# Optimization experiments

Hardware: AMD Instinct MI355X
Metric: run time of the kernel (lower is better)

The kernel has to match this reference:

```python
import jax, jax.numpy as jnp
import numpy as np
from jax import lax

B, C, T, S = 32, 122, 500, 13
WID, EMB, PROJ = 80, 8, 1024
HID = 768  # (H=1)*(W=96)*(E=8) after CNN
EPS = 1e-5
DN = ('NCHW', 'OIHW', 'NCHW')


def setup_inputs() -> dict:
    key = jax.random.key(0)
    ks = jax.random.split(key, 24)
    f32 = jnp.float32
    def n(k, shape, scale):
        return (jax.random.normal(k, shape, dtype=f32) * scale).astype(f32)
    return {
        'x': jax.random.normal(ks[0], (B, C, T), dtype=f32),
        'subject_ids': jax.random.randint(ks[1], (B,), 0, S, dtype=jnp.int32),
        'W_sub': n(ks[2], (S, T, T), 0.04),      # nn.Linear(500,500) weight per subject
        'b_sub': n(ks[3], (S, T), 0.02),
        'conv1_w': n(ks[4], (WID, 1, 1, 5), 0.3),
        'conv1_b': n(ks[5], (WID,), 0.02),
        'bn1_g': 1.0 + n(ks[6], (WID,), 0.1),
        'bn1_b': n(ks[7], (WID,), 0.1),
        'bn1_m': n(ks[8], (WID,), 0.1),
        'bn1_v': 0.5 + jax.random.uniform(ks[9], (WID,), dtype=f32),
        'conv2_w': n(ks[10], (WID, WID, C, 1), 0.01),
        'conv2_b': n(ks[11], (WID,), 0.02),
        'bn2_g': 1.0 + n(ks[12], (WID,), 0.1),
        'bn2_b': n(ks[13], (WID,), 0.1),
        'bn2_m': n(ks[14], (WID,), 0.1),
        'bn2_v': 0.5 + jax.random.uniform(ks[15], (WID,), dtype=f32),
        'proj_w': n(ks[16], (EMB, WID, 1, 1), 0.1),
        'proj_b': n(ks[17], (EMB,), 0.02),
        'mlp1_w': n(ks[18], (PROJ, HID), 0.03),
        'mlp1_b': n(ks[19], (PROJ,), 0.02),
        'mlp2_w': n(ks[20], (PROJ, PROJ), 0.03),
        'mlp2_b': n(ks[21], (PROJ,), 0.02),
        'ln_g': 1.0 + n(ks[22], (PROJ,), 0.05),
        'ln_b': n(ks[23], (PROJ,), 0.05),
    }


def _bn(h, g, b, m, v):
    # eval-mode BatchNorm2d over channel axis 1
    scale = (g / jnp.sqrt(v + EPS))[None, :, None, None]
    shift = (b - m * g / jnp.sqrt(v + EPS))[None, :, None, None]
    return h * scale + shift


def _forward(x, subject_ids, W_sub, b_sub, conv1_w, conv1_b, bn1_g, bn1_b, bn1_m, bn1_v,
             conv2_w, conv2_b, bn2_g, bn2_b, bn2_m, bn2_v, proj_w, proj_b,
             mlp1_w, mlp1_b, mlp2_w, mlp2_b, ln_g, ln_b):
    # --- per-subject routing: gather each sample's Linear(500,500) and apply ---
    Wg = W_sub[subject_ids]                       # [B,T,T] (out,in)
    bg = b_sub[subject_ids]                       # [B,T]
    out = jnp.einsum('bcs,bts->bct', x, Wg) + bg[:, None, :]
    # --- spatio-temporal CNN (eval mode: dropout = identity) ---
    h = out[:, None, :, :]                        # [B,1,C,T]
    h = lax.conv_general_dilated(h, conv1_w, (1, 1), 'VALID', dimension_numbers=DN)
    h = h + conv1_b[None, :, None, None]          # [B,80,122,496]
    h = lax.reduce_window(h, 0.0, lax.add, (1, 1, 1, 17), (1, 1, 1, 5), 'VALID') / 17.0  # [B,80,122,96]
    h = jax.nn.elu(_bn(h, bn1_g, bn1_b, bn1_m, bn1_v))
    h = lax.conv_general_dilated(h, conv2_w, (1, 1), 'VALID', dimension_numbers=DN)
    h = h + conv2_b[None, :, None, None]          # [B,80,1,96]
    h = jax.nn.elu(_bn(h, bn2_g, bn2_b, bn2_m, bn2_v))
    h = lax.conv_general_dilated(h, proj_w, (1, 1), 'VALID', dimension_numbers=DN)
    h = h + proj_b[None, :, None, None]           # [B,8,1,96]
    z = jnp.transpose(h, (0, 2, 3, 1)).reshape(h.shape[0], -1)  # [B,768]
    # --- MLP projector: Linear -> Residual(GELU+Linear) -> LayerNorm ---
    z1 = z @ mlp1_w.T + mlp1_b                    # [B,1024]
    r = jax.nn.gelu(z1, approximate=False) @ mlp2_w.T + mlp2_b
    y = z1 + r
    mu = jnp.mean(y, axis=-1, keepdims=True)
    var = jnp.var(y, axis=-1, keepdims=True)
    return (y - mu) / jnp.sqrt(var + EPS) * ln_g + ln_b


def reference(x, subject_ids, W_sub, b_sub, conv1_w, conv1_b, bn1_g, bn1_b, bn1_m, bn1_v,
              conv2_w, conv2_b, bn2_g, bn2_b, bn2_m, bn2_v, proj_w, proj_b,
              mlp1_w, mlp1_b, mlp2_w, mlp2_b, ln_g, ln_b):
    return _forward(x, subject_ids, W_sub, b_sub, conv1_w, conv1_b, bn1_g, bn1_b, bn1_m, bn1_v,
                    conv2_w, conv2_b, bn2_g, bn2_b, bn2_m, bn2_v, proj_w, proj_b,
                    mlp1_w, mlp1_b, mlp2_w, mlp2_b, ln_g, ln_b)
```

## Files before the change

### kernel.cpp

```cpp
#include <hip/hip_runtime.h>
#include <math.h>

#define BB 32
#define CC 122
#define TT 500
#define SS 13
#define WID 80
#define EMB 8
#define PROJ 1024
#define HID 768
#define TP 96
#define EPSF 1e-5f
#define KP 9760
#define KBN 305
#define KSPLIT 16

typedef float f32x4 __attribute__((ext_vector_type(4)));
typedef __bf16 bf16x8 __attribute__((ext_vector_type(8)));
typedef unsigned short u16x8 __attribute__((ext_vector_type(8)));
union BF8 { u16x8 u; bf16x8 b; };

__device__ __forceinline__ unsigned short f2bf(float f) {
    union { float f; unsigned u; } v; v.f = f;
    unsigned r = v.u + 0x7FFFu + ((v.u >> 16) & 1u);
    return (unsigned short)(r >> 16);
}

__device__ __forceinline__ float eluf(float x) {
    return x > 0.f ? x : __expf(x) - 1.f;
}

#define OFF_E    ((size_t)0)
#define OFF_XB   ((size_t)1952000)
#define OFF_WB   ((size_t)3000576)
#define OFF_W2P  ((size_t)4704512)
#define OFF_P    ((size_t)5094912)
#define OFF_PART ((size_t)20086272)
#define OFF_Z    ((size_t)24018432)
#define OFF_Z1   ((size_t)24030720)
#define OFF_G    ((size_t)24063488)
#define OFF_Y    ((size_t)24079872)
#define OFF_W1B  ((size_t)24112640)
#define OFF_W2B  ((size_t)24505856)
#define OFF_WCB  ((size_t)25030144)
#define OFF_B1F  ((size_t)25031424)
#define OFF_SC2  ((size_t)25031504)
#define OFF_SH2  ((size_t)25031584)

#define NPK_X  (2097152)
#define NPK_W  (3407872)
#define NPK_W2 (780800)
#define NPK_M1 (786432)
#define NPK_M2 (1048576)
#define NPK_TOT (NPK_X + NPK_W + NPK_W2 + NPK_M1 + NPK_M2)

__global__ __launch_bounds__(256) void k_pack(const float* __restrict__ x,
                                              const float* __restrict__ W_sub,
                                              const float* __restrict__ conv2_w,
                                              const float* __restrict__ mlp1_w,
                                              const float* __restrict__ mlp2_w,
                                              const float* __restrict__ conv1_w, const float* __restrict__ conv1_b,
                                              const float* __restrict__ g1, const float* __restrict__ b1,
                                              const float* __restrict__ m1, const float* __restrict__ v1,
                                              const float* __restrict__ conv2_b, const float* __restrict__ g2,
                                              const float* __restrict__ b2, const float* __restrict__ m2,
                                              const float* __restrict__ v2,
                                              unsigned short* __restrict__ xb,
                                              unsigned short* __restrict__ wb,
                                              unsigned short* __restrict__ w2p,
                                              unsigned short* __restrict__ w1b,
                                              unsigned short* __restrict__ w2b,
                                              unsigned short* __restrict__ wcb, float* __restrict__ bias1f,
                                              float* __restrict__ scale2, float* __restrict__ shift2f) {
    if (blockIdx.x == 0) {
        int o = threadIdx.x;
        if (o < WID) {
            float s1 = g1[o] * rsqrtf(v1[o] + EPSF);
            float sh1 = b1[o] - m1[o] * s1;
            #pragma unroll
            for (int d = 0; d < 21; d++) {
                int klo = d - 16; if (klo < 0) klo = 0;
                int khi = d;      if (khi > 4) khi = 4;
                float acc = 0.f;
                for (int k = klo; k <= khi; k++) acc += conv1_w[o*5 + k];
                wcb[o*32 + d] = f2bf(acc * s1 * (1.f/17.f));
            }
            #pragma unroll
            for (int d = 21; d < 32; d++) wcb[o*32 + d] = 0;
            bias1f[o] = conv1_b[o] * s1 + sh1;
            float s2 = g2[o] * rsqrtf(v2[o] + EPSF);
            scale2[o] = s2;
            shift2f[o] = conv2_b[o] * s2 + (b2[o] - m2[o] * s2);
        }
    }
    size_t idx = (size_t)blockIdx.x * 256 + threadIdx.x;
    if (idx >= (size_t)NPK_TOT) return;
    if (idx < NPK_X) {
        int s = idx & 511, c = (idx >> 9) & 127, b = idx >> 16;
        float v = (c < CC && s < TT) ? x[((size_t)b * CC + c) * TT + s] : 0.f;
        xb[idx] = f2bf(v);
    } else if (idx < NPK_X + NPK_W) {
        size_t j = idx - NPK_X;
        int s = j & 511, t = (j >> 9) & 511, sub = j >> 18;
        float v = (t < TT && s < TT) ? W_sub[((size_t)sub * TT + t) * TT + s] : 0.f;
        wb[j] = f2bf(v);
    } else if (idx < NPK_X + NPK_W + NPK_W2) {
        size_t j = idx - NPK_X - NPK_W;
        int o = (int)(j / KP);
        int k = (int)(j % KP);
        int c = k / WID, op = k % WID;
        w2p[j] = f2bf(conv2_w[((size_t)(o * WID + op)) * CC + c]);
    } else if (idx < NPK_X + NPK_W + NPK_W2 + NPK_M1) {
        size_t j = idx - NPK_X - NPK_W - NPK_W2;
        w1b[j] = f2bf(mlp1_w[j]);
    } else {
        size_t j = idx - NPK_X - NPK_W - NPK_W2 - NPK_M1;
        w2b[j] = f2bf(mlp2_w[j]);
    }
}

__global__ __launch_bounds__(256) void k_einsum(const unsigned short* __restrict__ xb,
                                                const unsigned short* __restrict__ wb,
                                                const int* __restrict__ sid,
                                                const float* __restrict__ b_sub,
                                                float* __restrict__ oute) {
    int t0 = blockIdx.x * 64, b = blockIdx.y;
    int s = sid[b];
    int tid = threadIdx.x, w = tid >> 6, lr = tid & 15, lg = (tid >> 4) & 3;
    const unsigned short* A0 = xb + ((size_t)(b * 128 + w * 32 + lr)) * 512 + 8 * lg;
    const unsigned short* Bb = wb + (size_t)s * 262144 + 8 * lg;
    f32x4 acc[2][4] = {};
    for (int kb = 0; kb < 512; kb += 32) {
        BF8 a0, a1;
        a0.u = *(const u16x8*)(A0 + kb);
        a1.u = *(const u16x8*)(A0 + 16 * 512 + kb);
        #pragma unroll
        for (int nt = 0; nt < 4; nt++) {
            BF8 bf; bf.u = *(const u16x8*)(Bb + (size_t)(t0 + nt * 16 + lr) * 512 + kb);
            acc[0][nt] = __builtin_amdgcn_mfma_f32_16x16x32_bf16(a0.b, bf.b, acc[0][nt], 0, 0, 0);
            acc[1][nt] = __builtin_amdgcn_mfma_f32_16x16x32_bf16(a1.b, bf.b, acc[1][nt], 0, 0, 0);
        }
    }
    const float* bg = b_sub + (size_t)s * TT;
    #pragma unroll
    for (int nt = 0; nt < 4; nt++) {
        int t = t0 + nt * 16 + lr;
        if (t < TT) {
            float bias = bg[t];
            #pragma unroll
            for (int mt = 0; mt < 2; mt++) {
                int crow = w * 32 + mt * 16 + 4 * lg;
                #pragma unroll
                for (int r = 0; r < 4; r++) {
                    int c = crow + r;
                    if (c < CC) oute[((size_t)b * CC + c) * TT + t] = acc[mt][nt][r] + bias;
                }
            }
        }
    }
}

__global__ __launch_bounds__(256) void k_fir2(const float* __restrict__ oute,
                                              const unsigned short* __restrict__ wcb,
                                              const float* __restrict__ b1f,
                                              unsigned short* __restrict__ p2) {
    __shared__ float e2[2][512];
    __shared__ unsigned short pt[96][164];
    int cp = blockIdx.x, b = blockIdx.y;
    int tid = threadIdx.x;
    int w = tid >> 6, lr = tid & 15, lg = (tid >> 4) & 3;
    if (tid < 250) {
        int cc = tid / 125, i = tid % 125;
        ((float4*)e2[cc])[i] = ((const float4*)(oute + ((size_t)b * CC + cp * 2 + cc) * TT))[i];
    }
    if (tid >= 232) {
        int j = tid - 232; int cc = j / 12, i = 500 + (j % 12);
        e2[cc][i] = 0.f;
    }
    BF8 af[5]; float4 bf4[5];
    #pragma unroll
    for (int ot = 0; ot < 5; ot++) {
        af[ot].u = *(const u16x8*)(wcb + (ot * 16 + lr) * 32 + 8 * lg);
        bf4[ot] = *(const float4*)(b1f + ot * 16 + 4 * lg);
    }
    __syncthreads();
    #pragma unroll
    for (int ui = 0; ui < 3; ui++) {
        int u = w + 4 * ui;
        int cc = u / 6, tt = u % 6;
        int t = tt * 16 + lr;
        const float* ew = e2[cc] + 5 * t + 8 * lg;
        BF8 bfr;
        #pragma unroll
        for (int j = 0; j < 8; j++) bfr.u[j] = f2bf(ew[j]);
        f32x4 acc[5] = {};
        #pragma unroll
        for (int ot = 0; ot < 5; ot++)
            acc[ot] = __builtin_amdgcn_mfma_f32_16x16x32_bf16(af[ot].b, bfr.b, acc[ot], 0, 0, 0);
        #pragma unroll
        for (int ot = 0; ot < 5; ot++) {
            union { unsigned short s[4]; uint2 v; } pk;
            #pragma unroll
            for (int r = 0; r < 4; r++) pk.s[r] = f2bf(eluf(acc[ot][r] + bf4[ot][r]));
            *(uint2*)&pt[t][cc * 80 + ot * 16 + 4 * lg] = pk.v;
        }
    }
    __syncthreads();
    const size_t base = ((size_t)b * KBN + 5 * (size_t)cp) * 3072;
    int q = 2 * tid;
    int l = q >> 3, jj = q & 7;
    int prow_lo = l & 15;
    int pcol_off = ((l >> 4) << 3) + jj;
    #pragma unroll
    for (int r = 0; r < 30; r++) {
        int kbl = r / 6, tt2 = r % 6;
        unsigned v = *(const unsigned*)&pt[tt2 * 16 + prow_lo][kbl * 32 + pcol_off];
        *(unsigned*)(p2 + base + (size_t)(kbl * 6 + tt2) * 512 + q) = v;
    }
}

__global__ __launch_bounds__(384) void k_conv2(const unsigned short* __restrict__ p2,
                                               const unsigned short* __restrict__ w2p,
                                               float* __restrict__ part) {
    int chunk = blockIdx.x, b = blockIdx.y;
    int tid = threadIdx.x, w = tid >> 6, l = tid & 63, lr = l & 15, lg = l >> 4;
    int kb0 = (chunk * KBN) / KSPLIT;
    int kb1 = ((chunk + 1) * KBN) / KSPLIT;
    const unsigned short* Bp = p2 + (size_t)b * KBN * 3072 + (size_t)w * 512 + (size_t)l * 8;
    const unsigned short* Arow = w2p + (size_t)lr * KP + 8 * lg;
    f32x4 acc[5] = {};
    for (int kb = kb0; kb < kb1; kb++) {
        BF8 bf; bf.u = *(const u16x8*)(Bp + (size_t)kb * 3072);
        int ko = kb * 32;
        #pragma unroll
        for (int mt = 0; mt < 5; mt++) {
            BF8 af; af.u = *(const u16x8*)(Arow + (size_t)mt * 16 * KP + ko);
            acc[mt] = __builtin_amdgcn_mfma_f32_16x16x32_bf16(af.b, bf.b, acc[mt], 0, 0, 0);
        }
    }
    float* pp = part + ((size_t)(chunk * BB + b) * WID) * TP;
    int t = w * 16 + lr;
    #pragma unroll
    for (int mt = 0; mt < 5; mt++) {
        int ob = mt * 16 + 4 * lg;
        #pragma unroll
        for (int r = 0; r < 4; r++)
            pp[(size_t)(ob + r) * TP + t] = acc[mt][r];
    }
}

__global__ __launch_bounds__(256) void k_redproj(const float* __restrict__ part,
                                                 const float* __restrict__ scale2,
                                                 const float* __restrict__ shift2f,
                                                 const float* __restrict__ pw,
                                                 const float* __restrict__ pb,
                                                 unsigned short* __restrict__ zbf) {
    __shared__ float ly[WID * TP];
    __shared__ float lw[EMB * WID];
    int b = blockIdx.x, tid = threadIdx.x;
    for (int i = tid; i < EMB * WID; i += 256) lw[i] = pw[i];
    for (int i = tid; i < WID * TP; i += 256) {
        float acc = 0.f;
        #pragma unroll
        for (int ks = 0; ks < KSPLIT; ks++)
            acc += part[(size_t)(ks * BB + b) * (WID * TP) + i];
        int o = i / TP;
        ly[i] = eluf(acc * scale2[o] + shift2f[o]);
    }
    __syncthreads();
    #pragma unroll
    for (int rep = 0; rep < 3; rep++) {
        int j = tid + 256 * rep;
        int e = j & 7, t = j >> 3;
        float acc = pb[e];
        #pragma unroll 10
        for (int o = 0; o < WID; o++) acc = fmaf(ly[o * TP + t], lw[e * WID + o], acc);
        zbf[(size_t)b * HID + j] = f2bf(acc);
    }
}

__global__ __launch_bounds__(256) void k_mlp1(const unsigned short* __restrict__ zbf,
                                              const unsigned short* __restrict__ w1b,
                                              const float* __restrict__ bias,
                                              float* __restrict__ z1,
                                              unsigned short* __restrict__ gbf) {
    __shared__ float accb[2][64][4];
    int tid = threadIdx.x, w = tid >> 6, l = tid & 63, lr = l & 15, lg = l >> 4;
    int mt = w & 1, kh = w >> 1;
    int pcol = blockIdx.x * 16 + lr;
    const unsigned short* wr = w1b + (size_t)pcol * HID + kh * 384 + 8 * lg;
    const unsigned short* za = zbf + (size_t)(mt * 16 + lr) * HID + kh * 384 + 8 * lg;
    f32x4 acc = {};
    for (int kb = 0; kb < 384; kb += 32) {
        BF8 bf; bf.u = *(const u16x8*)(wr + kb);
        BF8 a;  a.u  = *(const u16x8*)(za + kb);
        acc = __builtin_amdgcn_mfma_f32_16x16x32_bf16(a.b, bf.b, acc, 0, 0, 0);
    }
    if (kh == 1) {
        #pragma unroll
        for (int r = 0; r < 4; r++) accb[mt][l][r] = acc[r];
    }
    __syncthreads();
    if (kh == 0) {
        float bs = bias[pcol];
        #pragma unroll
        for (int r = 0; r < 4; r++) {
            int row = mt * 16 + 4 * lg + r;
            float v = acc[r] + accb[mt][l][r] + bs;
            z1[(size_t)row * PROJ + pcol] = v;
            gbf[(size_t)row * PROJ + pcol] = f2bf(0.5f * v * (1.f + erff(v * 0.70710678118654752f)));
        }
    }
}

__global__ __launch_bounds__(256) void k_mlp2(const unsigned short* __restrict__ gbf,
                                              const float* __restrict__ z1,
                                              const unsigned short* __restrict__ w2b,
                                              const float* __restrict__ bias,
                                              float* __restrict__ y) {
    __shared__ float accb[2][64][4];
    int tid = threadIdx.x, w = tid >> 6, l = tid & 63, lr = l & 15, lg = l >> 4;
    int mt = w & 1, kh = w >> 1;
    int q = blockIdx.x * 16 + lr;
    const unsigned short* wr = w2b + (size_t)q * PROJ + kh * 512 + 8 * lg;
    const unsigned short* ga = gbf + (size_t)(mt * 16 + lr) * PROJ + kh * 512 + 8 * lg;
    f32x4 acc = {};
    for (int kb = 0; kb < 512; kb += 32) {
        BF8 bf; bf.u = *(const u16x8*)(wr + kb);
        BF8 a;  a.u  = *(const u16x8*)(ga + kb);
        acc = __builtin_amdgcn_mfma_f32_16x16x32_bf16(a.b, bf.b, acc, 0, 0, 0);
    }
    if (kh == 1) {
        #pragma unroll
        for (int r = 0; r < 4; r++) accb[mt][l][r] = acc[r];
    }
    __syncthreads();
    if (kh == 0) {
        float bs = bias[q];
        #pragma unroll
        for (int r = 0; r < 4; r++) {
            int row = mt * 16 + 4 * lg + r;
            y[(size_t)row * PROJ + q] = acc[r] + accb[mt][l][r] + bs + z1[(size_t)row * PROJ + q];
        }
    }
}

__global__ __launch_bounds__(256) void k_ln(const float* __restrict__ y,
                                            const float* __restrict__ lg,
                                            const float* __restrict__ lb,
                                            float* __restrict__ out) {
    int b = blockIdx.x, tid = threadIdx.x;
    const float4* yr = (const float4*)(y + (size_t)b * PROJ);
    float4 v = yr[tid];
    float s  = v.x + v.y + v.z + v.w;
    float sq = v.x*v.x + v.y*v.y + v.z*v.z + v.w*v.w;
    #pragma unroll
    for (int off = 32; off > 0; off >>= 1) {
        s  += __shfl_down(s, off);
        sq += __shfl_down(sq, off);
    }
    __shared__ float ss[4], ssq[4];
    int wv = tid >> 6, lane = tid & 63;
    if (lane == 0) { ss[wv] = s; ssq[wv] = sq; }
    __syncthreads();
    __shared__ float smu, sinv;
    if (tid == 0) {
        float Sm = ss[0] + ss[1] + ss[2] + ss[3];
        float Sq = ssq[0] + ssq[1] + ssq[2] + ssq[3];
        float mu = Sm * (1.f / PROJ);
        float var = Sq * (1.f / PROJ) - mu * mu;
        smu = mu;
        sinv = rsqrtf(var + EPSF);
    }
    __syncthreads();
    float mu = smu, inv = sinv;
    float4 g4 = ((const float4*)lg)[tid];
    float4 b4 = ((const float4*)lb)[tid];
    float4 o4;
    o4.x = (v.x - mu) * inv * g4.x + b4.x;
    o4.y = (v.y - mu) * inv * g4.y + b4.y;
    o4.z = (v.z - mu) * inv * g4.z + b4.z;
    o4.w = (v.w - mu) * inv * g4.w + b4.w;
    ((float4*)(out + (size_t)b * PROJ))[tid] = o4;
}

extern "C" void kernel_launch(void* const* d_in, const int* in_sizes, int n_in,
                              void* d_out, int out_size, void* d_ws, size_t ws_size,
                              hipStream_t stream) {
    const float* x        = (const float*)d_in[0];
    const int*   sid      = (const int*)  d_in[1];
    const float* W_sub    = (const float*)d_in[2];
    const float* b_sub    = (const float*)d_in[3];
    const float* conv1_w  = (const float*)d_in[4];
    const float* conv1_b  = (const float*)d_in[5];
    const float* bn1_g    = (const float*)d_in[6];
    const float* bn1_b    = (const float*)d_in[7];
    const float* bn1_m    = (const float*)d_in[8];
    const float* bn1_v    = (const float*)d_in[9];
    const float* conv2_w  = (const float*)d_in[10];
    const float* conv2_b  = (const float*)d_in[11];
    const float* bn2_g    = (const float*)d_in[12];
    const float* bn2_b    = (const float*)d_in[13];
    const float* bn2_m    = (const float*)d_in[14];
    const float* bn2_v    = (const float*)d_in[15];
    const float* proj_w   = (const float*)d_in[16];
    const float* proj_b   = (const float*)d_in[17];
    const float* mlp1_w   = (const float*)d_in[18];
    const float* mlp1_b   = (const float*)d_in[19];
    const float* mlp2_w   = (const float*)d_in[20];
    const float* mlp2_b   = (const float*)d_in[21];
    const float* ln_g     = (const float*)d_in[22];
    const float* ln_b     = (const float*)d_in[23];
    float* out = (float*)d_out;
    float* ws  = (float*)d_ws;

    float* ws_e    = ws + OFF_E;
    unsigned short* ws_xb  = (unsigned short*)(ws + OFF_XB);
    unsigned short* ws_wb  = (unsigned short*)(ws + OFF_WB);
    unsigned short* ws_w2p = (unsigned short*)(ws + OFF_W2P);
    unsigned short* ws_p2  = (unsigned short*)(ws + OFF_P);
    float* ws_part = ws + OFF_PART;
    unsigned short* ws_zbf = (unsigned short*)(ws + OFF_Z);
    float* ws_z1   = ws + OFF_Z1;
    unsigned short* ws_gbf = (unsigned short*)(ws + OFF_G);
    float* ws_y    = ws + OFF_Y;
    unsigned short* ws_w1b = (unsigned short*)(ws + OFF_W1B);
    unsigned short* ws_w2b = (unsigned short*)(ws + OFF_W2B);
    unsigned short* ws_wcb = (unsigned short*)(ws + OFF_WCB);
    float* ws_b1f  = ws + OFF_B1F;
    float* ws_sc2  = ws + OFF_SC2;
    float* ws_sh2  = ws + OFF_SH2;

    hipLaunchKernelGGL(k_pack, dim3((NPK_TOT + 255) / 256), dim3(256), 0, stream,
                       x, W_sub, conv2_w, mlp1_w, mlp2_w,
                       conv1_w, conv1_b, bn1_g, bn1_b, bn1_m, bn1_v,
                       conv2_b, bn2_g, bn2_b, bn2_m, bn2_v,
                       ws_xb, ws_wb, ws_w2p, ws_w1b, ws_w2b,
                       ws_wcb, ws_b1f, ws_sc2, ws_sh2);

    hipLaunchKernelGGL(k_einsum, dim3(8, BB), dim3(256), 0, stream,
                       ws_xb, ws_wb, sid, b_sub, ws_e);

    hipLaunchKernelGGL(k_fir2, dim3(CC / 2, BB), dim3(256), 0, stream,
                       ws_e, ws_wcb, ws_b1f, ws_p2);

    hipLaunchKernelGGL(k_conv2, dim3(KSPLIT, BB), dim3(384), 0, stream,
                       ws_p2, ws_w2p, ws_part);

    hipLaunchKernelGGL(k_redproj, dim3(BB), dim3(256), 0, stream,
                       ws_part, ws_sc2, ws_sh2, proj_w, proj_b, ws_zbf);

    hipLaunchKernelGGL(k_mlp1, dim3(PROJ / 16), dim3(256), 0, stream,
                       ws_zbf, ws_w1b, mlp1_b, ws_z1, ws_gbf);

    hipLaunchKernelGGL(k_mlp2, dim3(PROJ / 16), dim3(256), 0, stream,
                       ws_gbf, ws_z1, ws_w2b, mlp2_b, ws_y);

    hipLaunchKernelGGL(k_ln, dim3(BB), dim3(256), 0, stream,
                       ws_y, ln_g, ln_b, out);
}
```

Measured before the change: 221.8 us.

## Fuse reduce/projection, MLP and LayerNorm tail into one kernel with grid barriers

```diff
diff --git a/kernel.cpp b/kernel.cpp
--- a/kernel.cpp
+++ b/kernel.cpp
@@ -14,6 +14,7 @@
 #define KP 9760
 #define KBN 305
 #define KSPLIT 16
+#define NTAIL 64
 
 typedef float f32x4 __attribute__((ext_vector_type(4)));
 typedef __bf16 bf16x8 __attribute__((ext_vector_type(8)));
@@ -37,7 +38,6 @@
 #define OFF_P    ((size_t)5094912)
 #define OFF_PART ((size_t)20086272)
 #define OFF_Z    ((size_t)24018432)
-#define OFF_Z1   ((size_t)24030720)
 #define OFF_G    ((size_t)24063488)
 #define OFF_Y    ((size_t)24079872)
 #define OFF_W1B  ((size_t)24112640)
@@ -46,6 +46,7 @@
 #define OFF_B1F  ((size_t)25031424)
 #define OFF_SC2  ((size_t)25031504)
 #define OFF_SH2  ((size_t)25031584)
+#define OFF_CNT  ((size_t)25031664)
 
 #define NPK_X  (2097152)
 #define NPK_W  (3407872)
@@ -71,9 +72,11 @@
                                               unsigned short* __restrict__ w1b,
                                               unsigned short* __restrict__ w2b,
                                               unsigned short* __restrict__ wcb, float* __restrict__ bias1f,
-                                              float* __restrict__ scale2, float* __restrict__ shift2f) {
+                                              float* __restrict__ scale2, float* __restrict__ shift2f,
+                                              unsigned* __restrict__ bar) {
     if (blockIdx.x == 0) {
         int o = threadIdx.x;
+        if (o < 8) bar[o] = 0u;
         if (o < WID) {
             float s1 = g1[o] * rsqrtf(v1[o] + EPSF);
             float sh1 = b1[o] - m1[o] * s1;
@@ -249,139 +252,153 @@
     }
 }
 
-__global__ __launch_bounds__(256) void k_redproj(const float* __restrict__ part,
-                                                 const float* __restrict__ scale2,
-                                                 const float* __restrict__ shift2f,
-                                                 const float* __restrict__ pw,
-                                                 const float* __restrict__ pb,
-                                                 unsigned short* __restrict__ zbf) {
+__device__ __forceinline__ void gbarrier(unsigned* ctr) {
+    __threadfence();
+    __syncthreads();
+    if (threadIdx.x == 0) {
+        atomicAdd(ctr, 1u);
+        while (atomicAdd(ctr, 0u) < NTAIL) {}
+    }
+    __syncthreads();
+    __threadfence();
+}
+
+__global__ __launch_bounds__(256) void k_tail(const float* __restrict__ part,
+                                              const float* __restrict__ scale2,
+                                              const float* __restrict__ shift2f,
+                                              const float* __restrict__ pw,
+                                              const float* __restrict__ pb,
+                                              const unsigned short* __restrict__ w1b,
+                                              const float* __restrict__ b1m,
+                                              const unsigned short* __restrict__ w2b,
+                                              const float* __restrict__ b2m,
+                                              const float* __restrict__ lg_,
+                                              const float* __restrict__ lb_,
+                                              unsigned short* __restrict__ zbf,
+                                              unsigned short* __restrict__ gbf,
+                                              float* __restrict__ y,
+                                              float* __restrict__ out,
+                                              unsigned* __restrict__ bar) {
     __shared__ float ly[WID * TP];
     __shared__ float lw[EMB * WID];
-    int b = blockIdx.x, tid = threadIdx.x;
-    for (int i = tid; i < EMB * WID; i += 256) lw[i] = pw[i];
-    for (int i = tid; i < WID * TP; i += 256) {
-        float acc = 0.f;
-        #pragma unroll
-        for (int ks = 0; ks < KSPLIT; ks++)
-            acc += part[(size_t)(ks * BB + b) * (WID * TP) + i];
-        int o = i / TP;
-        ly[i] = eluf(acc * scale2[o] + shift2f[o]);
-    }
-    __syncthreads();
-    #pragma unroll
-    for (int rep = 0; rep < 3; rep++) {
-        int j = tid + 256 * rep;
-        int e = j & 7, t = j >> 3;
-        float acc = pb[e];
-        #pragma unroll 10
-        for (int o = 0; o < WID; o++) acc = fmaf(ly[o * TP + t], lw[e * WID + o], acc);
-        zbf[(size_t)b * HID + j] = f2bf(acc);
-    }
-}
-
-__global__ __launch_bounds__(256) void k_mlp1(const unsigned short* __restrict__ zbf,
-                                              const unsigned short* __restrict__ w1b,
-                                              const float* __restrict__ bias,
-                                              float* __restrict__ z1,
-                                              unsigned short* __restrict__ gbf) {
     __shared__ float accb[2][64][4];
     int tid = threadIdx.x, w = tid >> 6, l = tid & 63, lr = l & 15, lg = l >> 4;
     int mt = w & 1, kh = w >> 1;
-    int pcol = blockIdx.x * 16 + lr;
-    const unsigned short* wr = w1b + (size_t)pcol * HID + kh * 384 + 8 * lg;
-    const unsigned short* za = zbf + (size_t)(mt * 16 + lr) * HID + kh * 384 + 8 * lg;
-    f32x4 acc = {};
-    for (int kb = 0; kb < 384; kb += 32) {
-        BF8 bf; bf.u = *(const u16x8*)(wr + kb);
-        BF8 a;  a.u  = *(const u16x8*)(za + kb);
-        acc = __builtin_amdgcn_mfma_f32_16x16x32_bf16(a.b, bf.b, acc, 0, 0, 0);
-    }
-    if (kh == 1) {
-        #pragma unroll
-        for (int r = 0; r < 4; r++) accb[mt][l][r] = acc[r];
-    }
-    __syncthreads();
-    if (kh == 0) {
-        float bs = bias[pcol];
-        #pragma unroll
-        for (int r = 0; r < 4; r++) {
-            int row = mt * 16 + 4 * lg + r;
-            float v = acc[r] + accb[mt][l][r] + bs;
-            z1[(size_t)row * PROJ + pcol] = v;
-            gbf[(size_t)row * PROJ + pcol] = f2bf(0.5f * v * (1.f + erff(v * 0.70710678118654752f)));
-        }
-    }
-}
-
-__global__ __launch_bounds__(256) void k_mlp2(const unsigned short* __restrict__ gbf,
-                                              const float* __restrict__ z1,
-                                              const unsigned short* __restrict__ w2b,
-                                              const float* __restrict__ bias,
-                                              float* __restrict__ y) {
-    __shared__ float accb[2][64][4];
-    int tid = threadIdx.x, w = tid >> 6, l = tid & 63, lr = l & 15, lg = l >> 4;
-    int mt = w & 1, kh = w >> 1;
-    int q = blockIdx.x * 16 + lr;
-    const unsigned short* wr = w2b + (size_t)q * PROJ + kh * 512 + 8 * lg;
-    const unsigned short* ga = gbf + (size_t)(mt * 16 + lr) * PROJ + kh * 512 + 8 * lg;
-    f32x4 acc = {};
-    for (int kb = 0; kb < 512; kb += 32) {
-        BF8 bf; bf.u = *(const u16x8*)(wr + kb);
-        BF8 a;  a.u  = *(const u16x8*)(ga + kb);
-        acc = __builtin_amdgcn_mfma_f32_16x16x32_bf16(a.b, bf.b, acc, 0, 0, 0);
-    }
-    if (kh == 1) {
-        #pragma unroll
-        for (int r = 0; r < 4; r++) accb[mt][l][r] = acc[r];
-    }
-    __syncthreads();
-    if (kh == 0) {
-        float bs = bias[q];
-        #pragma unroll
-        for (int r = 0; r < 4; r++) {
-            int row = mt * 16 + 4 * lg + r;
-            y[(size_t)row * PROJ + q] = acc[r] + accb[mt][l][r] + bs + z1[(size_t)row * PROJ + q];
-        }
-    }
-}
-
-__global__ __launch_bounds__(256) void k_ln(const float* __restrict__ y,
-                                            const float* __restrict__ lg,
-                                            const float* __restrict__ lb,
-                                            float* __restrict__ out) {
-    int b = blockIdx.x, tid = threadIdx.x;
-    const float4* yr = (const float4*)(y + (size_t)b * PROJ);
-    float4 v = yr[tid];
-    float s  = v.x + v.y + v.z + v.w;
-    float sq = v.x*v.x + v.y*v.y + v.z*v.z + v.w*v.w;
-    #pragma unroll
-    for (int off = 32; off > 0; off >>= 1) {
-        s  += __shfl_down(s, off);
-        sq += __shfl_down(sq, off);
-    }
-    __shared__ float ss[4], ssq[4];
-    int wv = tid >> 6, lane = tid & 63;
-    if (lane == 0) { ss[wv] = s; ssq[wv] = sq; }
-    __syncthreads();
-    __shared__ float smu, sinv;
-    if (tid == 0) {
-        float Sm = ss[0] + ss[1] + ss[2] + ss[3];
-        float Sq = ssq[0] + ssq[1] + ssq[2] + ssq[3];
-        float mu = Sm * (1.f / PROJ);
-        float var = Sq * (1.f / PROJ) - mu * mu;
-        smu = mu;
-        sinv = rsqrtf(var + EPSF);
-    }
-    __syncthreads();
-    float mu = smu, inv = sinv;
-    float4 g4 = ((const float4*)lg)[tid];
-    float4 b4 = ((const float4*)lb)[tid];
-    float4 o4;
-    o4.x = (v.x - mu) * inv * g4.x + b4.x;
-    o4.y = (v.y - mu) * inv * g4.y + b4.y;
-    o4.z = (v.z - mu) * inv * g4.z + b4.z;
-    o4.w = (v.w - mu) * inv * g4.w + b4.w;
-    ((float4*)(out + (size_t)b * PROJ))[tid] = o4;
+    float z1r[4];
+
+    if (blockIdx.x < BB) {
+        int b = blockIdx.x;
+        for (int i = tid; i < EMB * WID; i += 256) lw[i] = pw[i];
+        for (int i = tid; i < WID * TP; i += 256) {
+            float acc = 0.f;
+            #pragma unroll
+            for (int ks = 0; ks < KSPLIT; ks++)
+                acc += part[(size_t)(ks * BB + b) * (WID * TP) + i];
+            int o = i / TP;
+            ly[i] = eluf(acc * scale2[o] + shift2f[o]);
+        }
+        __syncthreads();
+        #pragma unroll
+        for (int rep = 0; rep < 3; rep++) {
+            int j = tid + 256 * rep;
+            int e = j & 7, t = j >> 3;
+            float acc = pb[e];
+            #pragma unroll 10
+            for (int o = 0; o < WID; o++) acc = fmaf(ly[o * TP + t], lw[e * WID + o], acc);
+            zbf[(size_t)b * HID + j] = f2bf(acc);
+        }
+    }
+    gbarrier(bar + 0);
+
+    {
+        int pcol = blockIdx.x * 16 + lr;
+        const unsigned short* wr = w1b + (size_t)pcol * HID + kh * 384 + 8 * lg;
+        const unsigned short* za = zbf + (size_t)(mt * 16 + lr) * HID + kh * 384 + 8 * lg;
+        f32x4 acc = {};
+        for (int kb = 0; kb < 384; kb += 32) {
+            BF8 bf; bf.u = *(const u16x8*)(wr + kb);
+            BF8 a;  a.u  = *(const u16x8*)(za + kb);
+            acc = __builtin_amdgcn_mfma_f32_16x16x32_bf16(a.b, bf.b, acc, 0, 0, 0);
+        }
+        if (kh == 1) {
+            #pragma unroll
+            for (int r = 0; r < 4; r++) accb[mt][l][r] = acc[r];
+        }
+        __syncthreads();
+        if (kh == 0) {
+            float bs = b1m[pcol];
+            #pragma unroll
+            for (int r = 0; r < 4; r++) {
+                int row = mt * 16 + 4 * lg + r;
+                float v = acc[r] + accb[mt][l][r] + bs;
+                z1r[r] = v;
+                gbf[(size_t)row * PROJ + pcol] = f2bf(0.5f * v * (1.f + erff(v * 0.70710678118654752f)));
+            }
+        }
+    }
+    gbarrier(bar + 1);
+
+    {
+        int q = blockIdx.x * 16 + lr;
+        const unsigned short* wr = w2b + (size_t)q * PROJ + kh * 512 + 8 * lg;
+        const unsigned short* ga = gbf + (size_t)(mt * 16 + lr) * PROJ + kh * 512 + 8 * lg;
+        f32x4 acc = {};
+        for (int kb = 0; kb < 512; kb += 32) {
+            BF8 bf; bf.u = *(const u16x8*)(wr + kb);
+            BF8 a;  a.u  = *(const u16x8*)(ga + kb);
+            acc = __builtin_amdgcn_mfma_f32_16x16x32_bf16(a.b, bf.b, acc, 0, 0, 0);
+        }
+        if (kh == 1) {
+            #pragma unroll
+            for (int r = 0; r < 4; r++) accb[mt][l][r] = acc[r];
+        }
+        __syncthreads();
+        if (kh == 0) {
+            float bs = b2m[q];
+            #pragma unroll
+            for (int r = 0; r < 4; r++) {
+                int row = mt * 16 + 4 * lg + r;
+                y[(size_t)row * PROJ + q] = acc[r] + accb[mt][l][r] + bs + z1r[r];
+            }
+        }
+    }
+    gbarrier(bar + 2);
+
+    if (blockIdx.x < BB) {
+        int b = blockIdx.x;
+        const float4* yr = (const float4*)(y + (size_t)b * PROJ);
+        float4 v = yr[tid];
+        float s  = v.x + v.y + v.z + v.w;
+        float sq = v.x*v.x + v.y*v.y + v.z*v.z + v.w*v.w;
+        #pragma unroll
+        for (int off = 32; off > 0; off >>= 1) {
+            s  += __shfl_down(s, off);
+            sq += __shfl_down(sq, off);
+        }
+        __shared__ float ss[4], ssq[4];
+        __shared__ float smu, sinv;
+        int wv = tid >> 6, lane = tid & 63;
+        if (lane == 0) { ss[wv] = s; ssq[wv] = sq; }
+        __syncthreads();
+        if (tid == 0) {
+            float Sm = ss[0] + ss[1] + ss[2] + ss[3];
+            float Sq = ssq[0] + ssq[1] + ssq[2] + ssq[3];
+            float mu = Sm * (1.f / PROJ);
+            float var = Sq * (1.f / PROJ) - mu * mu;
+            smu = mu;
+            sinv = rsqrtf(var + EPSF);
+        }
+        __syncthreads();
+        float mu = smu, inv = sinv;
+        float4 g4 = ((const float4*)lg_)[tid];
+        float4 b4 = ((const float4*)lb_)[tid];
+        float4 o4;
+        o4.x = (v.x - mu) * inv * g4.x + b4.x;
+        o4.y = (v.y - mu) * inv * g4.y + b4.y;
+        o4.z = (v.z - mu) * inv * g4.z + b4.z;
+        o4.w = (v.w - mu) * inv * g4.w + b4.w;
+        ((float4*)(out + (size_t)b * PROJ))[tid] = o4;
+    }
 }
 
 extern "C" void kernel_launch(void* const* d_in, const int* in_sizes, int n_in,
@@ -421,7 +438,6 @@
     unsigned short* ws_p2  = (unsigned short*)(ws + OFF_P);
     float* ws_part = ws + OFF_PART;
     unsigned short* ws_zbf = (unsigned short*)(ws + OFF_Z);
-    float* ws_z1   = ws + OFF_Z1;
     unsigned short* ws_gbf = (unsigned short*)(ws + OFF_G);
     float* ws_y    = ws + OFF_Y;
     unsigned short* ws_w1b = (unsigned short*)(ws + OFF_W1B);
@@ -430,13 +446,14 @@
     float* ws_b1f  = ws + OFF_B1F;
     float* ws_sc2  = ws + OFF_SC2;
     float* ws_sh2  = ws + OFF_SH2;
+    unsigned* ws_bar = (unsigned*)(ws + OFF_CNT);
 
     hipLaunchKernelGGL(k_pack, dim3((NPK_TOT + 255) / 256), dim3(256), 0, stream,
                        x, W_sub, conv2_w, mlp1_w, mlp2_w,
                        conv1_w, conv1_b, bn1_g, bn1_b, bn1_m, bn1_v,
                        conv2_b, bn2_g, bn2_b, bn2_m, bn2_v,
                        ws_xb, ws_wb, ws_w2p, ws_w1b, ws_w2b,
-                       ws_wcb, ws_b1f, ws_sc2, ws_sh2);
+                       ws_wcb, ws_b1f, ws_sc2, ws_sh2, ws_bar);
 
     hipLaunchKernelGGL(k_einsum, dim3(8, BB), dim3(256), 0, stream,
                        ws_xb, ws_wb, sid, b_sub, ws_e);
@@ -447,15 +464,8 @@
     hipLaunchKernelGGL(k_conv2, dim3(KSPLIT, BB), dim3(384), 0, stream,
                        ws_p2, ws_w2p, ws_part);
 
-    hipLaunchKernelGGL(k_redproj, dim3(BB), dim3(256), 0, stream,
-                       ws_part, ws_sc2, ws_sh2, proj_w, proj_b, ws_zbf);
-
-    hipLaunchKernelGGL(k_mlp1, dim3(PROJ / 16), dim3(256), 0, stream,
-                       ws_zbf, ws_w1b, mlp1_b, ws_z1, ws_gbf);
-
-    hipLaunchKernelGGL(k_mlp2, dim3(PROJ / 16), dim3(256), 0, stream,
-                       ws_gbf, ws_z1, ws_w2b, mlp2_b, ws_y);
-
-    hipLaunchKernelGGL(k_ln, dim3(BB), dim3(256), 0, stream,
-                       ws_y, ln_g, ln_b, out);
-}
+    hipLaunchKernelGGL(k_tail, dim3(NTAIL), dim3(256), 0, stream,
+                       ws_part, ws_sc2, ws_sh2, proj_w, proj_b,
+                       ws_w1b, mlp1_b, ws_w2b, mlp2_b, ln_g, ln_b,
+                       ws_zbf, ws_gbf, ws_y, out, ws_bar);
+}
```

Measured after the change: 247.1 us. 1.11x slower.
